# Optimization experiments

Hardware: AMD Instinct MI355X
Metric: run time of the kernel (lower is better)

Reference implementation:

```python
import jax, jax.numpy as jnp
import numpy as np

B, S, D_IN = 2, 2048, 2048
NUM_HEADS, NUM_KV_GROUPS, HEAD_DIM = 32, 8, 64
GROUP_SIZE = NUM_HEADS // NUM_KV_GROUPS  # 4
D_OUT = NUM_HEADS * HEAD_DIM  # 2048


def setup_inputs() -> dict:
    key = jax.random.key(0)
    k1, k2, k3, k4, k5 = jax.random.split(key, 5)
    scale_in = 1.0 / np.sqrt(D_IN)
    scale_out = 1.0 / np.sqrt(D_OUT)
    return {
        "x": jax.random.normal(k1, (B, S, D_IN), dtype=jnp.float32),
        # Linear weights stored torch-style as (out_features, in_features); y = x @ W.T
        "Wq": jax.random.uniform(k2, (D_OUT, D_IN), minval=-scale_in, maxval=scale_in, dtype=jnp.float32),
        "Wk": jax.random.uniform(k3, (NUM_KV_GROUPS * HEAD_DIM, D_IN), minval=-scale_in, maxval=scale_in, dtype=jnp.float32),
        "Wv": jax.random.uniform(k4, (NUM_KV_GROUPS * HEAD_DIM, D_IN), minval=-scale_in, maxval=scale_in, dtype=jnp.float32),
        "Wo": jax.random.uniform(k5, (D_IN, D_OUT), minval=-scale_out, maxval=scale_out, dtype=jnp.float32),
    }


def reference(x, Wq, Wk, Wv, Wo):
    b, s, _ = x.shape
    # Projections
    q = (x @ Wq.T).reshape(b, s, NUM_KV_GROUPS, GROUP_SIZE, HEAD_DIM)  # [b,s,g,r,d]
    k = (x @ Wk.T).reshape(b, s, NUM_KV_GROUPS, HEAD_DIM)              # [b,s,g,d]
    v = (x @ Wv.T).reshape(b, s, NUM_KV_GROUPS, HEAD_DIM)
    # Scores: broadcast each KV group over its group of query heads
    # (equivalent to repeat_interleave of K/V along head dim)
    scores = jnp.einsum("bqgrd,bkgd->bgrqk", q, k) / np.sqrt(HEAD_DIM).astype(jnp.float32)
    causal = jnp.tril(jnp.ones((s, s), dtype=bool))  # True = keep
    scores = jnp.where(causal, scores, jnp.finfo(scores.dtype).min)
    attn = jax.nn.softmax(scores, axis=-1)  # [b,g,r,q,k]
    ctx = jnp.einsum("bgrqk,bkgd->bqgrd", attn, v).reshape(b, s, D_OUT)
    out = ctx @ Wo.T
    # new_kv_cache (un-expanded keys/values, layout [b, g, s, d])
    keys = k.transpose(0, 2, 1, 3)
    values = v.transpose(0, 2, 1, 3)
    return out, (keys, values)
```

## Files before the change

kernel.cpp:

```cpp
#include <hip/hip_runtime.h>


#define B_   2
#define S_   2048
#define DIN  2048
#define NH   32
#define NKV  8
#define HD   64
#define DOUT 2048
#define NQKV 3072

#define QSCALE 0.18033688f

typedef short bf16x8 __attribute__((ext_vector_type(8)));
typedef short bf16x4 __attribute__((ext_vector_type(4)));
typedef float f32x4  __attribute__((ext_vector_type(4)));

__device__ __forceinline__ unsigned short f2bf(float f) {
  unsigned int u = __float_as_uint(f);
  u += 0x7fff + ((u >> 16) & 1);
  return (unsigned short)(u >> 16);
}

__device__ __forceinline__ f32x4 mfma16(bf16x4 a, bf16x4 b, f32x4 c) {
#if __has_builtin(__builtin_amdgcn_mfma_f32_16x16x16bf16_1k)
  return __builtin_amdgcn_mfma_f32_16x16x16bf16_1k(a, b, c, 0, 0, 0);
#else
  asm volatile("v_mfma_f32_16x16x16_bf16 %0, %1, %2, %0" : "+v"(c) : "v"(a), "v"(b));
  return c;
#endif
}

__device__ __forceinline__ void gld_lds16(const void* gptr, void* lptr) {
  __builtin_amdgcn_global_load_lds(
      (const __attribute__((address_space(1))) unsigned int*)gptr,
      (__attribute__((address_space(3))) unsigned int*)lptr,
      16, 0, 0);
}

__global__ __launch_bounds__(256) void cvt_all(
    const float* __restrict__ x,  const float* __restrict__ Wq,
    const float* __restrict__ Wk, const float* __restrict__ Wv,
    const float* __restrict__ Wo,
    unsigned short* __restrict__ xbf, unsigned short* __restrict__ wqkv,
    unsigned short* __restrict__ wobf) {
  int i = blockIdx.x * blockDim.x + threadIdx.x;
  const float* src; unsigned short* dst; int off;
  if (i < 2097152)      { src = x;  dst = xbf;                  off = i; }
  else if (i < 3145728) { src = Wq; dst = wqkv;                 off = i - 2097152; }
  else if (i < 3407872) { src = Wk; dst = wqkv + 2048 * 2048;   off = i - 3145728; }
  else if (i < 3670016) { src = Wv; dst = wqkv + 2560 * 2048;   off = i - 3407872; }
  else                  { src = Wo; dst = wobf;                 off = i - 3670016; }
  float4 f = ((const float4*)src)[off];
  ushort4 o;
  o.x = f2bf(f.x); o.y = f2bf(f.y); o.z = f2bf(f.z); o.w = f2bf(f.w);
  ((ushort4*)dst)[off] = o;
}

template <int MODE>
__global__ __launch_bounds__(256) void gemm_bt(
    const unsigned short* __restrict__ A,
    const unsigned short* __restrict__ Bm,
    int K,
    unsigned short* __restrict__ qbf,
    unsigned short* __restrict__ kbf,
    unsigned short* __restrict__ vtbf,
    float* __restrict__ kout,
    float* __restrict__ vout,
    float* __restrict__ cout) {
  __shared__ unsigned short As[8192];
  __shared__ unsigned short Bs[8192];
  const int tid  = threadIdx.x;
  const int lane = tid & 63;
  const int wave = tid >> 6;
  const int wm   = wave & 1;
  const int wn   = wave >> 1;
  const int quad = lane >> 4;
  const int r16  = lane & 15;
  const int crow = lane >> 3;
  const int ccol = (lane & 7) * 8;

  const int aRowBase = blockIdx.y * 128;
  const int bRowBase = blockIdx.x * 128;

  f32x4 zero = {0.f, 0.f, 0.f, 0.f};
  f32x4 acc[4][4];
#pragma unroll
  for (int i = 0; i < 4; ++i)
#pragma unroll
    for (int j = 0; j < 4; ++j) acc[i][j] = zero;

  auto stage = [&](int k0) {
#pragma unroll
    for (int i = 0; i < 4; ++i) {
      const int seg = wave * 4 + i;
      const int row = seg * 8 + crow;
      gld_lds16(A  + (size_t)(aRowBase + row) * K + k0 + ccol, &As[seg * 512]);
      gld_lds16(Bm + (size_t)(bRowBase + row) * K + k0 + ccol, &Bs[seg * 512]);
    }
  };

  for (int k0 = 0; k0 < K; k0 += 64) {
    stage(k0);
    __syncthreads();
#pragma unroll
    for (int kk = 0; kk < 2; ++kk) {
      bf16x8 af[4], bfr[4];
#pragma unroll
      for (int mt = 0; mt < 4; ++mt)
        af[mt] = *(const bf16x8*)(&As[(wm * 64 + mt * 16 + r16) * 64 + kk * 32 + quad * 8]);
#pragma unroll
      for (int nt = 0; nt < 4; ++nt)
        bfr[nt] = *(const bf16x8*)(&Bs[(wn * 64 + nt * 16 + r16) * 64 + kk * 32 + quad * 8]);
#pragma unroll
      for (int mt = 0; mt < 4; ++mt)
#pragma unroll
        for (int nt = 0; nt < 4; ++nt)
          acc[mt][nt] = __builtin_amdgcn_mfma_f32_16x16x32_bf16(af[mt], bfr[nt], acc[mt][nt], 0, 0, 0);
    }
    __syncthreads();
  }

#pragma unroll
  for (int mt = 0; mt < 4; ++mt) {
#pragma unroll
    for (int nt = 0; nt < 4; ++nt) {
      const int rowb = aRowBase + wm * 64 + mt * 16 + quad * 4;
      const int col  = bRowBase + wn * 64 + nt * 16 + r16;
#pragma unroll
      for (int reg = 0; reg < 4; ++reg) {
        const float v = acc[mt][nt][reg];
        const int m = rowb + reg;
        if (MODE == 1) {
          cout[(size_t)m * DOUT + col] = v;
        } else {
          if (col < 2048) {
            qbf[(size_t)m * DOUT + col] = f2bf(v * QSCALE);
          } else if (col < 2560) {
            const int gg = (col - 2048) >> 6, d = col & 63;
            const int b = m >> 11, s = m & 2047;
            const size_t idx = ((size_t)(b * NKV + gg) * S_ + s) * HD + d;
            kbf[idx]  = f2bf(v);
            kout[idx] = v;
          } else {
            const int gg = (col - 2560) >> 6, d = col & 63;
            const int b = m >> 11, s = m & 2047;
            vtbf[((size_t)(b * NKV + gg) * HD + d) * S_ + s]  = f2bf(v);
            vout[((size_t)(b * NKV + gg) * S_ + s) * HD + d] = v;
          }
        }
      }
    }
  }
}

__global__ __launch_bounds__(512, 4) void attn_kernel(
    const unsigned short* __restrict__ Q,
    const unsigned short* __restrict__ Kb,
    const unsigned short* __restrict__ VT,
    unsigned short* __restrict__ ctx) {
  __shared__ unsigned short Kbuf[2][4096];
  __shared__ unsigned short Vbuf[2][4096];

  const int tid  = threadIdx.x;
  const int lane = tid & 63;
  const int wave = tid >> 6;
  const int grp  = wave >> 2;
  const int hw   = wave & 3;
  const int quad = lane >> 4;
  const int r16  = lane & 15;
  const int g    = blockIdx.y;
  const int b    = blockIdx.z;
  const int h    = g * 4 + hw;
  const int pairI = blockIdx.x;
  const int q0     = grp ? pairI * 32 : (63 - pairI) * 32;
  const int nT_own = grp ? pairI / 2 + 1 : (63 - pairI) / 2 + 1;
  const int nTa    = (63 - pairI) / 2 + 1;

  const unsigned short* Kh  = Kb + (size_t)(b * NKV + g) * S_ * HD;
  const unsigned short* VTh = VT + (size_t)(b * NKV + g) * HD * S_;

  const int srow   = lane >> 3;
  const int schunk = (lane & 7) ^ srow;

  bf16x8 aq[2][2];
#pragma unroll
  for (int mt = 0; mt < 2; ++mt)
#pragma unroll
    for (int kk = 0; kk < 2; ++kk)
      aq[mt][kk] = *(const bf16x8*)(Q + (size_t)(b * S_ + q0 + mt * 16 + r16) * DOUT +
                                    h * HD + kk * 32 + quad * 8);

  bf16x4 ones4;
#pragma unroll
  for (int i = 0; i < 4; ++i) ones4[i] = (short)0x3F80;

  f32x4 zero = {0.f, 0.f, 0.f, 0.f};
  f32x4 o[2][4];
  f32x4 l[2];
#pragma unroll
  for (int mt = 0; mt < 2; ++mt) {
    l[mt] = zero;
#pragma unroll
    for (int dt = 0; dt < 4; ++dt) o[mt][dt] = zero;
  }

  auto stage = [&](int buf, int kt) {
    const int kbase = kt * 64;
    gld_lds16(Kh + (size_t)(kbase + wave * 8 + srow) * HD + schunk * 8,
              &Kbuf[buf][wave * 512]);
    gld_lds16(VTh + (size_t)(wave * 8 + srow) * S_ + kbase + schunk * 8,
              &Vbuf[buf][wave * 512]);
  };

  stage(0, 0);
  __syncthreads();

  for (int kt = 0; kt < nTa; ++kt) {
    const int buf = kt & 1;
    if (kt + 1 < nTa) stage(buf ^ 1, kt + 1);

    if (kt < nT_own) {
      bf16x8 bk[4][2];
#pragma unroll
      for (int nt = 0; nt < 4; ++nt)
#pragma unroll
        for (int kk = 0; kk < 2; ++kk) {
          const int seg = nt * 2 + (r16 >> 3), r = r16 & 7;
          const int slot = (kk * 4 + quad) ^ r;
          bk[nt][kk] = *(const bf16x8*)&Kbuf[buf][seg * 512 + r * 64 + slot * 8];
        }

      const bool last = (kt == nT_own - 1);
#pragma unroll
      for (int mt = 0; mt < 2; ++mt) {
        f32x4 st[4];
#pragma unroll
        for (int nt = 0; nt < 4; ++nt) st[nt] = zero;
#pragma unroll
        for (int kk = 0; kk < 2; ++kk)
#pragma unroll
          for (int nt = 0; nt < 4; ++nt)
            st[nt] = __builtin_amdgcn_mfma_f32_16x16x32_bf16(bk[nt][kk], aq[mt][kk], st[nt], 0, 0, 0);

        bf16x4 pf[4];
#pragma unroll
        for (int nt = 0; nt < 4; ++nt) {
#pragma unroll
          for (int r = 0; r < 4; ++r) {
            float s = st[nt][r];
            if (last) {
              const int key = kt * 64 + nt * 16 + quad * 4 + r;
              const int row = q0 + mt * 16 + r16;
              if (key > row) s = -1e38f;
            }
            const float p = __builtin_amdgcn_exp2f(s);
            pf[nt][r] = (short)(__float_as_uint(p) >> 16);
          }
        }
#pragma unroll
        for (int nt = 0; nt < 4; ++nt) l[mt] = mfma16(pf[nt], ones4, l[mt]);
#pragma unroll
        for (int dt = 0; dt < 4; ++dt) {
          const int seg = dt * 2 + (r16 >> 3), r = r16 & 7;
#pragma unroll
          for (int nt = 0; nt < 4; ++nt) {
            const int slot = (nt * 2 + (quad >> 1)) ^ r;
            bf16x4 bv = *(const bf16x4*)&Vbuf[buf][seg * 512 + r * 64 + slot * 8 + (quad & 1) * 4];
            o[mt][dt] = mfma16(pf[nt], bv, o[mt][dt]);
          }
        }
      }
    }

    __syncthreads();
  }

#pragma unroll
  for (int mt = 0; mt < 2; ++mt) {
    f32x4 rl;
#pragma unroll
    for (int r = 0; r < 4; ++r) rl[r] = __builtin_amdgcn_rcpf(l[mt][r]);
#pragma unroll
    for (int dt = 0; dt < 4; ++dt)
#pragma unroll
      for (int r = 0; r < 4; ++r) {
        const int qq = q0 + mt * 16 + quad * 4 + r;
        ctx[(size_t)(b * S_ + qq) * DOUT + h * HD + dt * 16 + r16] =
            f2bf(o[mt][dt][r] * rl[r]);
      }
  }
}

extern "C" void kernel_launch(void* const* d_in, const int* in_sizes, int n_in,
                              void* d_out, int out_size, void* d_ws, size_t ws_size,
                              hipStream_t stream) {
  const float* x  = (const float*)d_in[0];
  const float* Wq = (const float*)d_in[1];
  const float* Wk = (const float*)d_in[2];
  const float* Wv = (const float*)d_in[3];
  const float* Wo = (const float*)d_in[4];

  float* out  = (float*)d_out;
  float* keys = out + (size_t)B_ * S_ * DOUT;
  float* vals = keys + (size_t)B_ * NKV * S_ * HD;

  unsigned short* xbf  = (unsigned short*)d_ws;
  unsigned short* wqkv = xbf  + (size_t)B_ * S_ * DIN;
  unsigned short* wobf = wqkv + (size_t)NQKV * DIN;
  unsigned short* qbf  = wobf + (size_t)DIN * DOUT;
  unsigned short* kbf  = qbf  + (size_t)B_ * S_ * DOUT;
  unsigned short* vtbf = kbf  + (size_t)B_ * NKV * S_ * HD;
  unsigned short* ctx  = vtbf + (size_t)B_ * NKV * S_ * HD;

  cvt_all<<<dim3(4718592 / 256), dim3(256), 0, stream>>>(x, Wq, Wk, Wv, Wo,
                                                         xbf, wqkv, wobf);

  gemm_bt<0><<<dim3(NQKV / 128, (B_ * S_) / 128), dim3(256), 0, stream>>>(
      xbf, wqkv, DIN, qbf, kbf, vtbf, keys, vals, nullptr);

  attn_kernel<<<dim3(32, NKV, B_), dim3(512), 0, stream>>>(qbf, kbf, vtbf, ctx);

  gemm_bt<1><<<dim3(DOUT / 128, (B_ * S_) / 128), dim3(256), 0, stream>>>(
      ctx, wobf, DOUT, nullptr, nullptr, nullptr, nullptr, nullptr, out);
}
```

Baseline: 328.7 us.

## Rewrite projection GEMMs as 8-wave double-buffered pipelined kernel with swizzled LDS

```diff
diff --git a/kernel.cpp b/kernel.cpp
--- a/kernel.cpp
+++ b/kernel.cpp
@@ -37,6 +37,15 @@
       (__attribute__((address_space(3))) unsigned int*)lptr,
       16, 0, 0);
 }
+
+#define BAR()                              \
+  do {                                     \
+    asm volatile("" ::: "memory");         \
+    __builtin_amdgcn_s_barrier();          \
+    asm volatile("" ::: "memory");         \
+  } while (0)
+
+#define VMCNT(n) asm volatile("s_waitcnt vmcnt(" #n ")" ::: "memory")
 
 __global__ __launch_bounds__(256) void cvt_all(
     const float* __restrict__ x,  const float* __restrict__ Wq,
@@ -57,8 +66,24 @@
   ((ushort4*)dst)[off] = o;
 }
 
-template <int MODE>
-__global__ __launch_bounds__(256) void gemm_bt(
+#define MMA_PHASE(MH, NH, BF)                                                   \
+  do {                                                                          \
+    __builtin_amdgcn_s_setprio(1);                                              \
+    _Pragma("unroll")                                                           \
+    for (int mr = 0; mr < 4; ++mr)                                              \
+      _Pragma("unroll")                                                         \
+      for (int nr = 0; nr < NR; ++nr)                                           \
+        _Pragma("unroll")                                                       \
+        for (int kk = 0; kk < 2; ++kk)                                          \
+          acc[(MH) * 4 + mr][(NH) * NR + nr] =                                  \
+              __builtin_amdgcn_mfma_f32_16x16x32_bf16(                          \
+                  af[mr][kk], BF[nr][kk], acc[(MH) * 4 + mr][(NH) * NR + nr],   \
+                  0, 0, 0);                                                     \
+    __builtin_amdgcn_s_setprio(0);                                              \
+  } while (0)
+
+template <int MODE, int BN, int NTN>
+__global__ __launch_bounds__(512, 2) void gemm8p(
     const unsigned short* __restrict__ A,
     const unsigned short* __restrict__ Bm,
     int K,
@@ -68,68 +93,149 @@
     float* __restrict__ kout,
     float* __restrict__ vout,
     float* __restrict__ cout) {
-  __shared__ unsigned short As[8192];
-  __shared__ unsigned short Bs[8192];
+  constexpr int NR = BN / 128;
+  constexpr int BHROW = BN / 2;
+  __shared__ unsigned short As[2][256 * 64];
+  __shared__ unsigned short Bs[2][BN * 64];
+
   const int tid  = threadIdx.x;
   const int lane = tid & 63;
   const int wave = tid >> 6;
-  const int wm   = wave & 1;
-  const int wn   = wave >> 1;
+  const int wm   = wave >> 2;
+  const int wn   = wave & 3;
   const int quad = lane >> 4;
   const int r16  = lane & 15;
-  const int crow = lane >> 3;
-  const int ccol = (lane & 7) * 8;
-
-  const int aRowBase = blockIdx.y * 128;
-  const int bRowBase = blockIdx.x * 128;
+
+  const int NT = K / 64;
+
+  const int nwg = gridDim.x;
+  const int id  = blockIdx.x;
+  const int sid = (id & 7) * (nwg >> 3) + (id >> 3);
+  const int by  = sid / NTN;
+  const int bx  = sid % NTN;
+  const int aRowBase = by * 256;
+  const int bColBase = bx * BN;
 
   f32x4 zero = {0.f, 0.f, 0.f, 0.f};
-  f32x4 acc[4][4];
-#pragma unroll
-  for (int i = 0; i < 4; ++i)
-#pragma unroll
-    for (int j = 0; j < 4; ++j) acc[i][j] = zero;
-
-  auto stage = [&](int k0) {
-#pragma unroll
-    for (int i = 0; i < 4; ++i) {
-      const int seg = wave * 4 + i;
-      const int row = seg * 8 + crow;
-      gld_lds16(A  + (size_t)(aRowBase + row) * K + k0 + ccol, &As[seg * 512]);
-      gld_lds16(Bm + (size_t)(bRowBase + row) * K + k0 + ccol, &Bs[seg * 512]);
+  f32x4 acc[8][2 * NR];
+#pragma unroll
+  for (int i = 0; i < 8; ++i)
+#pragma unroll
+    for (int j = 0; j < 2 * NR; ++j) acc[i][j] = zero;
+
+  auto stageA = [&](int dbuf, int h, int t) {
+    const int tt = t < NT ? t : NT - 1;
+    const int k0 = tt * 64;
+#pragma unroll
+    for (int i = 0; i < 2; ++i) {
+      const int chunk = (i * 8 + wave) * 64 + lane;
+      const int row = chunk >> 3;
+      const int slot = chunk & 7;
+      const int gc = (slot ^ (row & 7)) * 8;
+      gld_lds16(A + (size_t)(aRowBase + h * 128 + row) * K + k0 + gc,
+                &As[dbuf][h * 8192 + (i * 8 + wave) * 512]);
     }
   };
-
-  for (int k0 = 0; k0 < K; k0 += 64) {
-    stage(k0);
-    __syncthreads();
-#pragma unroll
-    for (int kk = 0; kk < 2; ++kk) {
-      bf16x8 af[4], bfr[4];
-#pragma unroll
-      for (int mt = 0; mt < 4; ++mt)
-        af[mt] = *(const bf16x8*)(&As[(wm * 64 + mt * 16 + r16) * 64 + kk * 32 + quad * 8]);
-#pragma unroll
-      for (int nt = 0; nt < 4; ++nt)
-        bfr[nt] = *(const bf16x8*)(&Bs[(wn * 64 + nt * 16 + r16) * 64 + kk * 32 + quad * 8]);
-#pragma unroll
-      for (int mt = 0; mt < 4; ++mt)
-#pragma unroll
-        for (int nt = 0; nt < 4; ++nt)
-          acc[mt][nt] = __builtin_amdgcn_mfma_f32_16x16x32_bf16(af[mt], bfr[nt], acc[mt][nt], 0, 0, 0);
+  auto stageB = [&](int dbuf, int h, int t) {
+    const int tt = t < NT ? t : NT - 1;
+    const int k0 = tt * 64;
+    if constexpr (BN == 256) {
+#pragma unroll
+      for (int i = 0; i < 2; ++i) {
+        const int chunk = (i * 8 + wave) * 64 + lane;
+        const int row = chunk >> 3;
+        const int slot = chunk & 7;
+        const int gc = (slot ^ (row & 7)) * 8;
+        gld_lds16(Bm + (size_t)(bColBase + h * 128 + row) * K + k0 + gc,
+                  &Bs[dbuf][h * 8192 + (i * 8 + wave) * 512]);
+      }
+    } else {
+      const int chunk = wave * 64 + lane;
+      const int row = chunk >> 3;
+      const int slot = chunk & 7;
+      const int gc = (slot ^ (row & 7)) * 8;
+      gld_lds16(Bm + (size_t)(bColBase + h * 64 + row) * K + k0 + gc,
+                &Bs[dbuf][h * 4096 + wave * 512]);
     }
-    __syncthreads();
+  };
+
+  bf16x8 af[4][2];
+  bf16x8 b0[NR][2];
+  bf16x8 b1[NR][2];
+
+  auto readA = [&](int sbuf, int mh) {
+#pragma unroll
+    for (int mr = 0; mr < 4; ++mr)
+#pragma unroll
+      for (int kk = 0; kk < 2; ++kk) {
+        const int row = mh * 128 + wm * 64 + mr * 16 + r16;
+        const int slot = (kk * 4 + quad) ^ (r16 & 7);
+        af[mr][kk] = *(const bf16x8*)&As[sbuf][row * 64 + slot * 8];
+      }
+  };
+  auto readB = [&](int sbuf, int nh, bf16x8 (&bf)[NR][2]) {
+#pragma unroll
+    for (int nr = 0; nr < NR; ++nr)
+#pragma unroll
+      for (int kk = 0; kk < 2; ++kk) {
+        const int row = nh * BHROW + wn * (BN / 8) + nr * 16 + r16;
+        const int slot = (kk * 4 + quad) ^ (r16 & 7);
+        bf[nr][kk] = *(const bf16x8*)&Bs[sbuf][row * 64 + slot * 8];
+      }
+  };
+
+  stageA(0, 0, 0);
+  stageA(0, 1, 0);
+  stageB(0, 0, 0);
+  stageB(0, 1, 0);
+  stageA(1, 0, 1);
+  if constexpr (BN == 256) VMCNT(4); else VMCNT(3);
+  BAR();
+
+  for (int t = 0; t < NT; ++t) {
+    const int buf = t & 1, nbuf = buf ^ 1;
+
+    readA(buf, 0);
+    readB(buf, 0, b0);
+    stageA(nbuf, 1, t + 1);
+    BAR();
+    MMA_PHASE(0, 0, b0);
+    VMCNT(4);
+    BAR();
+
+    readB(buf, 1, b1);
+    stageB(nbuf, 0, t + 1);
+    BAR();
+    MMA_PHASE(0, 1, b1);
+    BAR();
+
+    readA(buf, 1);
+    stageB(nbuf, 1, t + 1);
+    BAR();
+    MMA_PHASE(1, 0, b0);
+    BAR();
+
+    stageA(buf, 0, t + 2);
+    BAR();
+    MMA_PHASE(1, 1, b1);
+    if constexpr (BN == 256) VMCNT(4); else VMCNT(3);
+    BAR();
   }
-
-#pragma unroll
-  for (int mt = 0; mt < 4; ++mt) {
-#pragma unroll
-    for (int nt = 0; nt < 4; ++nt) {
-      const int rowb = aRowBase + wm * 64 + mt * 16 + quad * 4;
-      const int col  = bRowBase + wn * 64 + nt * 16 + r16;
+  VMCNT(0);
+
+#pragma unroll
+  for (int mi = 0; mi < 8; ++mi) {
+    const int mh = mi >> 2, mr = mi & 3;
+#pragma unroll
+    for (int ni = 0; ni < 2 * NR; ++ni) {
+      const int nh = ni / NR, nr = ni % NR;
+      const int rowb = aRowBase + mh * 128 + wm * 64 + mr * 16 + quad * 4;
+      const int col  = bColBase +
+                       (BN == 256 ? nh * 128 + wn * 32 + nr * 16
+                                  : nh * 64 + wn * 16) + r16;
 #pragma unroll
       for (int reg = 0; reg < 4; ++reg) {
-        const float v = acc[mt][nt][reg];
+        const float v = acc[mi][ni][reg];
         const int m = rowb + reg;
         if (MODE == 1) {
           cout[(size_t)m * DOUT + col] = v;
@@ -316,11 +422,11 @@
   cvt_all<<<dim3(4718592 / 256), dim3(256), 0, stream>>>(x, Wq, Wk, Wv, Wo,
                                                          xbf, wqkv, wobf);
 
-  gemm_bt<0><<<dim3(NQKV / 128, (B_ * S_) / 128), dim3(256), 0, stream>>>(
+  gemm8p<0, 256, 12><<<dim3(192), dim3(512), 0, stream>>>(
       xbf, wqkv, DIN, qbf, kbf, vtbf, keys, vals, nullptr);
 
   attn_kernel<<<dim3(32, NKV, B_), dim3(512), 0, stream>>>(qbf, kbf, vtbf, ctx);
 
-  gemm_bt<1><<<dim3(DOUT / 128, (B_ * S_) / 128), dim3(256), 0, stream>>>(
+  gemm8p<1, 128, 16><<<dim3(256), dim3(512), 0, stream>>>(
       ctx, wobf, DOUT, nullptr, nullptr, nullptr, nullptr, nullptr, out);
 }
```

After: 320.2 us. 1.03x faster.
